# Kernel optimization log

Measured on AMD Instinct MI355X. Metric: run time of the kernel, lower is better.

Reference implementation:

```python
import jax, jax.numpy as jnp
import numpy as np

# ---- static problem configuration (matches init_kwargs) ----
N_PAIRS = 256
NODES_PER_GRAPH = 64
EDGES_PER_GRAPH = 200
MAX_EDGES = 256            # max_edge_set_size
N_GRAPHS = 2 * N_PAIRS     # query/corpus interleaved
N_NODES = N_GRAPHS * NODES_PER_GRAPH
N_EDGES = N_GRAPHS * EDGES_PER_GRAPH
NODE_DIM = 16
EDGE_DIM = 16
H = 128                    # node_state_dim
E_ENC = 64                 # encoded edge feature dim
MSG = 256                  # edge_hidden_sizes[-1] = 2*H (GMN GRU convention)
SK = 32                    # sinkhorn_feature_dim
PROP_STEPS = 5
SK_ITERS = 20
TEMP = 0.1


def setup_inputs() -> dict:
    key = jax.random.key(0)
    ks = jax.random.split(key, 16)
    node_features = jax.random.normal(ks[0], (N_NODES, NODE_DIM), jnp.float32)
    edge_features = jax.random.normal(ks[1], (N_EDGES, EDGE_DIM), jnp.float32)
    # edges are grouped per graph (graph g owns edges [g*E, (g+1)*E)) and
    # endpoints stay inside graph g's node range, as get_graph_features assumes
    offs = np.repeat(np.arange(N_GRAPHS) * NODES_PER_GRAPH, EDGES_PER_GRAPH)
    rng = np.random.default_rng(0)
    from_idx = jnp.asarray(offs + rng.integers(0, NODES_PER_GRAPH, N_EDGES), jnp.int32)
    to_idx = jnp.asarray(offs + rng.integers(0, NODES_PER_GRAPH, N_EDGES), jnp.int32)

    def lin(k, i, o):
        return jax.random.normal(k, (i, o), jnp.float32) / np.sqrt(i).astype(np.float32)

    p = dict(
        enc_node_w=lin(ks[2], NODE_DIM, H), enc_node_b=jnp.zeros((H,), jnp.float32),
        enc_edge_w=lin(ks[3], EDGE_DIM, E_ENC), enc_edge_b=jnp.zeros((E_ENC,), jnp.float32),
        msg_w1=lin(ks[4], 2 * H + E_ENC, MSG), msg_b1=jnp.zeros((MSG,), jnp.float32),
        msg_w2=lin(ks[5], MSG, MSG), msg_b2=jnp.zeros((MSG,), jnp.float32),
        rmsg_w1=lin(ks[6], 2 * H + E_ENC, MSG), rmsg_b1=jnp.zeros((MSG,), jnp.float32),
        rmsg_w2=lin(ks[7], MSG, MSG), rmsg_b2=jnp.zeros((MSG,), jnp.float32),
        gru_w_ih=lin(ks[8], MSG, 3 * H), gru_b_ih=jnp.zeros((3 * H,), jnp.float32),
        gru_w_hh=lin(ks[9], H, 3 * H), gru_b_hh=jnp.zeros((3 * H,), jnp.float32),
        sk_w1=lin(ks[10], MSG, SK), sk_b1=jnp.zeros((SK,), jnp.float32),
        sk_w2=lin(ks[11], SK, SK), sk_b2=jnp.zeros((SK,), jnp.float32),
    )
    return {"node_features": node_features, "edge_features": edge_features,
            "from_idx": from_idx, "to_idx": to_idx, **p}


def _mlp2(x, w1, b1, w2, b2):
    # Linear -> ReLU -> Linear (GMN MLP: no activation after last layer)
    return jax.nn.relu(x @ w1 + b1) @ w2 + b2


def reference(node_features, edge_features, from_idx, to_idx,
              enc_node_w, enc_node_b, enc_edge_w, enc_edge_b,
              msg_w1, msg_b1, msg_w2, msg_b2,
              rmsg_w1, rmsg_b1, rmsg_w2, rmsg_b2,
              gru_w_ih, gru_b_ih, gru_w_hh, gru_b_hh,
              sk_w1, sk_b1, sk_w2, sk_b2):
    # ---- GraphEncoder (single-layer MLPs) ----
    h = node_features @ enc_node_w + enc_node_b          # [N_NODES, H]
    e = edge_features @ enc_edge_w + enc_edge_b          # [N_EDGES, E_ENC]

    def edge_msgs(h):
        s, d = h[from_idx], h[to_idx]                    # gathers [N_EDGES, H]
        fwd = _mlp2(jnp.concatenate([s, d, e], axis=1), msg_w1, msg_b1, msg_w2, msg_b2)
        rev = _mlp2(jnp.concatenate([d, s, e], axis=1), rmsg_w1, rmsg_b1, rmsg_w2, rmsg_b2)
        return fwd, rev                                  # [N_EDGES, MSG] each

    # ---- propagation loop: gather -> edge MLP -> scatter -> GRU update ----
    for _ in range(PROP_STEPS):
        fwd, rev = edge_msgs(h)
        agg = (jax.ops.segment_sum(fwd, to_idx, num_segments=N_NODES)
               + jax.ops.segment_sum(rev, from_idx, num_segments=N_NODES))  # [N_NODES, MSG]
        gi = agg @ gru_w_ih + gru_b_ih                   # [N_NODES, 3H]
        gh = h @ gru_w_hh + gru_b_hh
        r = jax.nn.sigmoid(gi[:, :H] + gh[:, :H])
        z = jax.nn.sigmoid(gi[:, H:2 * H] + gh[:, H:2 * H])
        n = jnp.tanh(gi[:, 2 * H:] + r * gh[:, 2 * H:])
        h = (1.0 - z) * n + z * h                        # torch GRU update

    # ---- propagation_messages: per-edge fwd + rev message ----
    fwd, rev = edge_msgs(h)
    e_final = fwd + rev                                  # [N_EDGES, MSG]

    # ---- split_and_stack: per-graph edge sets padded to MAX_EDGES ----
    stacked = jnp.pad(e_final.reshape(N_GRAPHS, EDGES_PER_GRAPH, MSG),
                      ((0, 0), (0, MAX_EDGES - EDGES_PER_GRAPH), (0, 0)))
    q, c = stacked[0::2], stacked[1::2]                  # [B, MAX_EDGES, MSG]

    # ---- sinkhorn feature MLP + size mask ----
    tq = _mlp2(q, sk_w1, sk_b1, sk_w2, sk_b2)            # [B, MAX_EDGES, SK]
    tc = _mlp2(c, sk_w1, sk_b1, sk_w2, sk_b2)
    mask = (jnp.arange(MAX_EDGES) < EDGES_PER_GRAPH).astype(jnp.float32)[None, :, None]
    mq, mc = mask * tq, mask * tc

    # ---- log-domain Sinkhorn ----
    la = jnp.einsum('bif,bjf->bij', mq, mc) / TEMP       # [B, MAX_EDGES, MAX_EDGES]
    for _ in range(SK_ITERS):
        la = la - jax.nn.logsumexp(la, axis=2, keepdims=True)
        la = la - jax.nn.logsumexp(la, axis=1, keepdims=True)
    plan = jnp.exp(la)

    # ---- feature_alignment_score: -sum relu(q - P @ c) ----
    return -jnp.sum(jax.nn.relu(q - jnp.einsum('bij,bjf->bif', plan, c)), axis=(1, 2))
```

## Files before the change

### kernel.cpp

```cpp
#include <hip/hip_runtime.h>
#include <math.h>

typedef __attribute__((ext_vector_type(4))) float f32x4;
typedef __attribute__((ext_vector_type(8))) short s16x8;
typedef __attribute__((ext_vector_type(4))) short s16x4;

#define NN 32768
#define NE 102400
#define HD 128
#define EED 64
#define MSGD 256
#define NG 512
#define EPG 200
#define NP 256
#define SKD 32

__device__ inline short f2bf(float x){
  union{float f; unsigned u;} z; z.f=x;
  unsigned r = (z.u + 0x7fffu + ((z.u>>16)&1u)) >> 16;
  return (short)r;
}
__device__ inline float bf2f(unsigned short u){
  union{unsigned u; float f;} z; z.u = ((unsigned)u)<<16; return z.f;
}
__device__ inline float frcp(float x){
  float r; asm("v_rcp_f32 %0, %1" : "=v"(r) : "v"(x)); return r;
}

__global__ void __launch_bounds__(256) k_enc_node(const float* __restrict__ nf,
    const float* __restrict__ W, const float* __restrict__ b,
    float* __restrict__ h, short* __restrict__ hb){
  __shared__ float Ws[16*128];
  int t = threadIdx.x;
  for (int i=t;i<16*128;i+=256) Ws[i]=W[i];
  __syncthreads();
  int node = blockIdx.x*2 + (t>>7);
  int f = t & 127;
  const float* x = nf + node*16;
  float acc = b[f];
  #pragma unroll
  for (int k=0;k<16;k++) acc = fmaf(x[k], Ws[k*128+f], acc);
  h[node*HD+f] = acc;
  hb[node*HD+f] = f2bf(acc);
}

__global__ void __launch_bounds__(256) k_enc_edge(const float* __restrict__ ef,
    const float* __restrict__ W, const float* __restrict__ b, short* __restrict__ eeb){
  __shared__ float Ws[16*64];
  int t = threadIdx.x;
  for (int i=t;i<16*64;i+=256) Ws[i]=W[i];
  __syncthreads();
  int edge = blockIdx.x*4 + (t>>6);
  int f = t & 63;
  const float* x = ef + edge*16;
  float acc = b[f];
  #pragma unroll
  for (int k=0;k<16;k++) acc = fmaf(x[k], Ws[k*64+f], acc);
  eeb[edge*EED+f] = f2bf(acc);
}

__global__ void __launch_bounds__(256) k_pack(const float* __restrict__ W,
    short* __restrict__ dst, int K, int N){
  int NT = N >> 4;
  int i = blockIdx.x*256 + threadIdx.x;
  if (i >= (K/32)*NT*64) return;
  int l = i & 63, tile = i >> 6;
  int nt = tile % NT, kt = tile / NT;
  int lr = l & 15, lq = l >> 4;
  s16x8 v;
  #pragma unroll
  for (int j=0;j<8;j++)
    v[j] = f2bf(W[(size_t)(kt*32 + lq*8 + j)*N + nt*16 + lr]);
  *((s16x8*)dst + i) = v;
}

__global__ void __launch_bounds__(256) k_csr_count(const int* __restrict__ fidx,
    const int* __restrict__ tidx, int* __restrict__ cur_in, int* __restrict__ cur_out){
  int e = blockIdx.x*256 + threadIdx.x;
  if (e >= NE) return;
  atomicAdd(&cur_in[tidx[e]], 1);
  atomicAdd(&cur_out[fidx[e]], 1);
}
__global__ void k_csr_scan(int* __restrict__ cur_in, int* __restrict__ start_in,
    int* __restrict__ cur_out, int* __restrict__ start_out){
  if (threadIdx.x) return;
  int g = blockIdx.x;
  int n0 = g*64, base = g*EPG;
  int run = base;
  for (int i=0;i<64;i++){ int c=cur_in[n0+i]; start_in[n0+i]=run; cur_in[n0+i]=run; run+=c; }
  run = base;
  for (int i=0;i<64;i++){ int c=cur_out[n0+i]; start_out[n0+i]=run; cur_out[n0+i]=run; run+=c; }
}
__global__ void __launch_bounds__(256) k_csr_fill(const int* __restrict__ fidx,
    const int* __restrict__ tidx, int* __restrict__ cur_in, int* __restrict__ cur_out,
    int* __restrict__ list_in, int* __restrict__ list_out){
  int e = blockIdx.x*256 + threadIdx.x;
  if (e >= NE) return;
  int p1 = atomicAdd(&cur_in[tidx[e]], 1);  list_in[p1] = e;
  int p2 = atomicAdd(&cur_out[fidx[e]], 1); list_out[p2] = e;
}

template<bool FIN>
__global__ void __launch_bounds__(512,4) k_msg(const short* __restrict__ hb,
    const short* __restrict__ eeb, const int* __restrict__ from_idx, const int* __restrict__ to_idx,
    const short* __restrict__ w1f, const float* __restrict__ b1f,
    const short* __restrict__ w2f, const float* __restrict__ b2f,
    const short* __restrict__ w1r, const float* __restrict__ b1r,
    const short* __restrict__ w2r, const float* __restrict__ b2r,
    short* __restrict__ mf, short* __restrict__ mr){
  __shared__ __align__(16) short Xs[64][328];
  __shared__ __align__(16) short Ys[64][264];
  __shared__ int sidx[64], didx[64];
  int t = threadIdx.x;
  int e0 = blockIdx.x*64;
  if (t < 64){ sidx[t]=from_idx[e0+t]; didx[t]=to_idx[e0+t]; }
  __syncthreads();
  for (int i=t; i<64*40; i+=512){
    int r = i/40, c8 = (i - r*40)*8;
    const short* src;
    if (c8 < 128)      src = hb + (size_t)sidx[r]*HD + c8;
    else if (c8 < 256) src = hb + (size_t)didx[r]*HD + (c8-128);
    else               src = eeb + (size_t)(e0+r)*EED + (c8-256);
    *(s16x8*)&Xs[r][c8] = *(const s16x8*)src;
  }
  __syncthreads();

  int wv = t>>6, l = t&63, lr = l&15, lq = l>>4;
  int cbase = wv*32;
  f32x4 fsv[4][2];

  for (int dir=0; dir<2; dir++){
    const s16x8* W1v = (const s16x8*)(dir ? w1r : w1f);
    const float* B1  = dir ? b1r : b1f;
    const s16x8* W2v = (const s16x8*)(dir ? w2r : w2f);
    const float* B2  = dir ? b2r : b2f;

    f32x4 acc[4][2];
    #pragma unroll
    for (int ct=0; ct<2; ct++){
      float bb = B1[cbase + ct*16 + lr];
      #pragma unroll
      for (int rt=0; rt<4; rt++) acc[rt][ct] = (f32x4){bb,bb,bb,bb};
    }
    {
      s16x8 a0[4], b0[2], b1[2];
      int sc0 = dir ? 4 : 0;
      #pragma unroll
      for (int rt=0;rt<4;rt++) a0[rt] = *(const s16x8*)&Xs[rt*16+lr][sc0*32 + lq*8];
      #pragma unroll
      for (int ct=0;ct<2;ct++) b0[ct] = W1v[(size_t)(0*16 + wv*2 + ct)*64 + l];
      #pragma unroll
      for (int ct=0;ct<2;ct++) b1[ct] = W1v[(size_t)(1*16 + wv*2 + ct)*64 + l];
      #pragma unroll
      for (int kt=0; kt<10; kt++){
        s16x8 an[4], bn[2];
        if (kt < 9){
          int sc = (dir && (kt+1)<8) ? ((kt+1)^4) : (kt+1);
          #pragma unroll
          for (int rt=0;rt<4;rt++) an[rt] = *(const s16x8*)&Xs[rt*16+lr][sc*32 + lq*8];
        }
        if (kt < 8){
          #pragma unroll
          for (int ct=0;ct<2;ct++) bn[ct] = W1v[(size_t)((kt+2)*16 + wv*2 + ct)*64 + l];
        }
        #pragma unroll
        for (int rt=0; rt<4; rt++)
          #pragma unroll
          for (int ct=0; ct<2; ct++)
            acc[rt][ct] = __builtin_amdgcn_mfma_f32_16x16x32_bf16(a0[rt], b0[ct], acc[rt][ct], 0,0,0);
        #pragma unroll
        for (int i=0;i<4;i++) a0[i]=an[i];
        #pragma unroll
        for (int i=0;i<2;i++){ b0[i]=b1[i]; b1[i]=bn[i]; }
      }
    }
    #pragma unroll
    for (int rt=0; rt<4; rt++)
      #pragma unroll
      for (int ct=0; ct<2; ct++)
        #pragma unroll
        for (int r=0; r<4; r++)
          Ys[rt*16 + lq*4 + r][cbase + ct*16 + lr] = f2bf(fmaxf(acc[rt][ct][r], 0.f));
    __syncthreads();

    f32x4 acc2[4][2];
    #pragma unroll
    for (int ct=0; ct<2; ct++){
      float bb = B2[cbase + ct*16 + lr];
      #pragma unroll
      for (int rt=0; rt<4; rt++) acc2[rt][ct] = (f32x4){bb,bb,bb,bb};
    }
    {
      s16x8 a0[4], b0[2], b1[2];
      #pragma unroll
      for (int rt=0;rt<4;rt++) a0[rt] = *(const s16x8*)&Ys[rt*16+lr][lq*8];
      #pragma unroll
      for (int ct=0;ct<2;ct++) b0[ct] = W2v[(size_t)(0*16 + wv*2 + ct)*64 + l];
      #pragma unroll
      for (int ct=0;ct<2;ct++) b1[ct] = W2v[(size_t)(1*16 + wv*2 + ct)*64 + l];
      #pragma unroll
      for (int kt=0; kt<8; kt++){
        s16x8 an[4], bn[2];
        if (kt < 7){
          #pragma unroll
          for (int rt=0;rt<4;rt++) an[rt] = *(const s16x8*)&Ys[rt*16+lr][(kt+1)*32 + lq*8];
        }
        if (kt < 6){
          #pragma unroll
          for (int ct=0;ct<2;ct++) bn[ct] = W2v[(size_t)((kt+2)*16 + wv*2 + ct)*64 + l];
        }
        #pragma unroll
        for (int rt=0; rt<4; rt++)
          #pragma unroll
          for (int ct=0; ct<2; ct++)
            acc2[rt][ct] = __builtin_amdgcn_mfma_f32_16x16x32_bf16(a0[rt], b0[ct], acc2[rt][ct], 0,0,0);
        #pragma unroll
        for (int i=0;i<4;i++) a0[i]=an[i];
        #pragma unroll
        for (int i=0;i<2;i++){ b0[i]=b1[i]; b1[i]=bn[i]; }
      }
    }
    if (!FIN){
      __syncthreads();
      #pragma unroll
      for (int rt=0; rt<4; rt++)
        #pragma unroll
        for (int ct=0; ct<2; ct++)
          #pragma unroll
          for (int r=0; r<4; r++)
            Ys[rt*16 + lq*4 + r][cbase + ct*16 + lr] = f2bf(acc2[rt][ct][r]);
      __syncthreads();
      short* dst = (dir ? mr : mf) + (size_t)e0*MSGD;
      for (int i=t; i<64*32; i+=512){
        int row = i>>5, c8 = (i&31)*8;
        *(s16x8*)&dst[(size_t)row*MSGD + c8] = *(const s16x8*)&Ys[row][c8];
      }
      __syncthreads();
    } else {
      if (dir==0){
        #pragma unroll
        for (int rt=0; rt<4; rt++)
          #pragma unroll
          for (int ct=0; ct<2; ct++) fsv[rt][ct] = acc2[rt][ct];
        __syncthreads();
      } else {
        __syncthreads();
        #pragma unroll
        for (int rt=0; rt<4; rt++)
          #pragma unroll
          for (int ct=0; ct<2; ct++)
            #pragma unroll
            for (int r=0; r<4; r++)
              Ys[rt*16 + lq*4 + r][cbase + ct*16 + lr] = f2bf(fsv[rt][ct][r] + acc2[rt][ct][r]);
        __syncthreads();
        short* dst = mf + (size_t)e0*MSGD;
        for (int i=t; i<64*32; i+=512){
          int row = i>>5, c8 = (i&31)*8;
          *(s16x8*)&dst[(size_t)row*MSGD + c8] = *(const s16x8*)&Ys[row][c8];
        }
      }
    }
  }
}

__global__ void __launch_bounds__(256) k_gather(const unsigned short* __restrict__ mf,
    const unsigned short* __restrict__ mr,
    const int* __restrict__ start_in, const int* __restrict__ end_in, const int* __restrict__ list_in,
    const int* __restrict__ start_out, const int* __restrict__ end_out, const int* __restrict__ list_out,
    short* __restrict__ aggb){
  int n = blockIdx.x*4 + (threadIdx.x>>6);
  int l = threadIdx.x & 63;
  float4 acc = {0.f,0.f,0.f,0.f};
  int s0 = start_in[n], e0 = end_in[n];
  for (int i=s0; i<e0; i++){
    int e = list_in[i];
    ushort4 v = *(const ushort4*)&mf[(size_t)e*MSGD + 4*l];
    acc.x += bf2f(v.x); acc.y += bf2f(v.y); acc.z += bf2f(v.z); acc.w += bf2f(v.w);
  }
  int s1 = start_out[n], e1 = end_out[n];
  for (int i=s1; i<e1; i++){
    int e = list_out[i];
    ushort4 v = *(const ushort4*)&mr[(size_t)e*MSGD + 4*l];
    acc.x += bf2f(v.x); acc.y += bf2f(v.y); acc.z += bf2f(v.z); acc.w += bf2f(v.w);
  }
  s16x4 o;
  o[0]=f2bf(acc.x); o[1]=f2bf(acc.y); o[2]=f2bf(acc.z); o[3]=f2bf(acc.w);
  *(s16x4*)&aggb[(size_t)n*MSGD + 4*l] = o;
}

__global__ void __launch_bounds__(512,4) k_gru(const float* __restrict__ h,
    const short* __restrict__ hb, const short* __restrict__ aggb,
    const short* __restrict__ wih_p, const float* __restrict__ bih,
    const short* __restrict__ whh_p, const float* __restrict__ bhh,
    float* __restrict__ hnew, short* __restrict__ hnewb){
  __shared__ __align__(16) short aggs[64][264];
  __shared__ __align__(16) short hs[64][136];
  int t = threadIdx.x;
  int n0 = blockIdx.x*64;
  for (int i=t; i<64*32; i+=512){
    int r = i>>5, c8 = (i&31)*8;
    *(s16x8*)&aggs[r][c8] = *(const s16x8*)&aggb[(size_t)(n0+r)*MSGD + c8];
  }
  for (int i=t; i<64*16; i+=512){
    int r = i>>4, c8 = (i&15)*8;
    *(s16x8*)&hs[r][c8] = *(const s16x8*)&hb[(size_t)(n0+r)*HD + c8];
  }
  __syncthreads();

  int wv = t>>6, l = t&63, lr = l&15, lq = l>>4;
  const s16x8* Wih_v = (const s16x8*)wih_p;
  const s16x8* Whh_v = (const s16x8*)whh_p;

  f32x4 gi[4][3], gh[4][3];
  #pragma unroll
  for (int ct=0; ct<3; ct++){
    int bcol = ct*128 + wv*16 + lr;
    float bi = bih[bcol], bh = bhh[bcol];
    #pragma unroll
    for (int rt=0; rt<4; rt++){
      gi[rt][ct] = (f32x4){bi,bi,bi,bi};
      gh[rt][ct] = (f32x4){bh,bh,bh,bh};
    }
  }
  for (int kt=0; kt<8; kt++){
    s16x8 af[4], bfr[3];
    #pragma unroll
    for (int rt=0; rt<4; rt++) af[rt] = *(const s16x8*)&aggs[rt*16+lr][kt*32 + lq*8];
    #pragma unroll
    for (int ct=0; ct<3; ct++)
      bfr[ct] = Wih_v[(size_t)(kt*24 + ct*8 + wv)*64 + l];
    #pragma unroll
    for (int rt=0; rt<4; rt++)
      #pragma unroll
      for (int ct=0; ct<3; ct++)
        gi[rt][ct] = __builtin_amdgcn_mfma_f32_16x16x32_bf16(af[rt], bfr[ct], gi[rt][ct], 0,0,0);
  }
  for (int kt=0; kt<4; kt++){
    s16x8 af[4], bfr[3];
    #pragma unroll
    for (int rt=0; rt<4; rt++) af[rt] = *(const s16x8*)&hs[rt*16+lr][kt*32 + lq*8];
    #pragma unroll
    for (int ct=0; ct<3; ct++)
      bfr[ct] = Whh_v[(size_t)(kt*24 + ct*8 + wv)*64 + l];
    #pragma unroll
    for (int rt=0; rt<4; rt++)
      #pragma unroll
      for (int ct=0; ct<3; ct++)
        gh[rt][ct] = __builtin_amdgcn_mfma_f32_16x16x32_bf16(af[rt], bfr[ct], gh[rt][ct], 0,0,0);
  }
  #pragma unroll
  for (int rt=0; rt<4; rt++)
    #pragma unroll
    for (int r=0; r<4; r++){
      int row = n0 + rt*16 + lq*4 + r;
      int col = wv*16 + lr;
      float rr = 1.f/(1.f + __expf(-(gi[rt][0][r] + gh[rt][0][r])));
      float zz = 1.f/(1.f + __expf(-(gi[rt][1][r] + gh[rt][1][r])));
      float gn = gi[rt][2][r] + rr*gh[rt][2][r];
      float nn = 1.f - 2.f/(__expf(2.f*gn) + 1.f);
      float hold = h[(size_t)row*HD + col];
      float hv = (1.f - zz)*nn + zz*hold;
      hnew[(size_t)row*HD + col] = hv;
      hnewb[(size_t)row*HD + col] = f2bf(hv);
    }
}

__global__ void __launch_bounds__(256,2) k_tall(const short* __restrict__ efb,
    const short* __restrict__ W1p, const float* __restrict__ b1,
    const short* __restrict__ W2p, const float* __restrict__ b2,
    float* __restrict__ tall){
  __shared__ __align__(16) short Xs[64][264];
  __shared__ __align__(16) short Ys[64][40];
  int t = threadIdx.x;
  int g = blockIdx.x>>2, r0 = (blockIdx.x&3)*64;
  for (int i=t; i<64*32; i+=256){
    int r = i>>5, c8 = (i&31)*8;
    int row = r0 + r;
    s16x8 v = (row < EPG) ? *(const s16x8*)&efb[((size_t)g*EPG + row)*MSGD + c8]
                          : (s16x8){0,0,0,0,0,0,0,0};
    *(s16x8*)&Xs[r][c8] = v;
  }
  __syncthreads();
  int wv = t>>6, l = t&63, lr = l&15, lq = l>>4;
  const s16x8* W1v = (const s16x8*)W1p;
  const s16x8* W2v = (const s16x8*)W2p;
  f32x4 acc[2];
  #pragma unroll
  for (int ct=0; ct<2; ct++){
    float bb = b1[ct*16 + lr];
    acc[ct] = (f32x4){bb,bb,bb,bb};
  }
  for (int kt=0; kt<8; kt++){
    s16x8 a = *(const s16x8*)&Xs[wv*16+lr][kt*32 + lq*8];
    #pragma unroll
    for (int ct=0; ct<2; ct++){
      s16x8 bfr = W1v[(size_t)(kt*2 + ct)*64 + l];
      acc[ct] = __builtin_amdgcn_mfma_f32_16x16x32_bf16(a, bfr, acc[ct], 0,0,0);
    }
  }
  #pragma unroll
  for (int ct=0; ct<2; ct++)
    #pragma unroll
    for (int r=0; r<4; r++)
      Ys[wv*16 + lq*4 + r][ct*16 + lr] = f2bf(fmaxf(acc[ct][r], 0.f));
  __syncthreads();
  f32x4 acc2[2];
  #pragma unroll
  for (int ct=0; ct<2; ct++){
    float bb = b2[ct*16 + lr];
    acc2[ct] = (f32x4){bb,bb,bb,bb};
  }
  {
    s16x8 a = *(const s16x8*)&Ys[wv*16+lr][lq*8];
    #pragma unroll
    for (int ct=0; ct<2; ct++){
      s16x8 bfr = W2v[(size_t)ct*64 + l];
      acc2[ct] = __builtin_amdgcn_mfma_f32_16x16x32_bf16(a, bfr, acc2[ct], 0,0,0);
    }
  }
  #pragma unroll
  for (int ct=0; ct<2; ct++)
    #pragma unroll
    for (int r=0; r<4; r++){
      int row = r0 + wv*16 + lq*4 + r;
      tall[((size_t)g*256 + row)*SKD + ct*16 + lr] = (row < EPG) ? acc2[ct][r] : 0.f;
    }
}

__global__ void __attribute__((amdgpu_waves_per_eu(4,4))) __launch_bounds__(1024)
k_sinkhorn(const float* __restrict__ tall, short* __restrict__ plan){
  __shared__ float tqs[256*32];
  __shared__ float tcsT[32*257];
  __shared__ float cv[256];
  __shared__ float psm[16][256];
  int p = blockIdx.x, t = threadIdx.x;
  int w = t>>6, l = t&63;
  int rbase = w*16;
  const float* tq = tall + (size_t)(2*p)*8192;
  const float* tc = tall + (size_t)(2*p+1)*8192;
  for (int i=t; i<8192; i+=1024){
    tqs[i] = tq[i];
    tcsT[(i&31)*257 + (i>>5)] = tc[i];
  }
  __syncthreads();
  float4 E[16];
  #pragma unroll
  for (int k=0; k<16; k++){
    float4 a = {0.f,0.f,0.f,0.f};
    for (int kk=0; kk<32; kk+=4){
      float4 c0 = *(const float4*)&tcsT[(kk+0)*257 + 4*l];
      float4 c1 = *(const float4*)&tcsT[(kk+1)*257 + 4*l];
      float4 c2 = *(const float4*)&tcsT[(kk+2)*257 + 4*l];
      float4 c3 = *(const float4*)&tcsT[(kk+3)*257 + 4*l];
      float4 q = *(const float4*)&tqs[(rbase+k)*32 + kk];
      a.x = fmaf(q.x,c0.x, fmaf(q.y,c1.x, fmaf(q.z,c2.x, fmaf(q.w,c3.x, a.x))));
      a.y = fmaf(q.x,c0.y, fmaf(q.y,c1.y, fmaf(q.z,c2.y, fmaf(q.w,c3.y, a.y))));
      a.z = fmaf(q.x,c0.z, fmaf(q.y,c1.z, fmaf(q.z,c2.z, fmaf(q.w,c3.z, a.z))));
      a.w = fmaf(q.x,c0.w, fmaf(q.y,c1.w, fmaf(q.z,c2.w, fmaf(q.w,c3.w, a.w))));
    }
    a.x *= 10.f; a.y *= 10.f; a.z *= 10.f; a.w *= 10.f;
    float m = fmaxf(fmaxf(a.x,a.y), fmaxf(a.z,a.w));
    #pragma unroll
    for (int off=32; off; off>>=1) m = fmaxf(m, __shfl_xor(m, off));
    float s = __expf(a.x-m)+__expf(a.y-m)+__expf(a.z-m)+__expf(a.w-m);
    #pragma unroll
    for (int off=32; off; off>>=1) s += __shfl_xor(s, off);
    float r = m + __logf(s);
    E[k].x = __expf(a.x - r); E[k].y = __expf(a.y - r);
    E[k].z = __expf(a.z - r); E[k].w = __expf(a.w - r);
  }

  for (int it=0; it<20; it++){
    float4 sm = {0.f,0.f,0.f,0.f};
    #pragma unroll
    for (int k=0;k<16;k++){
      sm.x += E[k].x; sm.y += E[k].y; sm.z += E[k].z; sm.w += E[k].w;
    }
    *(float4*)&psm[w][4*l] = sm;
    __syncthreads();
    if (t < 256){
      float s = psm[0][t];
      #pragma unroll
      for (int ww=1; ww<16; ww++) s += psm[ww][t];
      cv[t] = frcp(s);
    }
    __syncthreads();
    float4 ic = *(const float4*)&cv[4*l];
    #pragma unroll
    for (int k=0;k<16;k++){
      E[k].x *= ic.x; E[k].y *= ic.y; E[k].z *= ic.z; E[k].w *= ic.w;
    }
    if (it < 19){
      #pragma unroll
      for (int k=0;k<16;k++){
        float s = E[k].x + E[k].y + E[k].z + E[k].w;
        #pragma unroll
        for (int off=32; off; off>>=1) s += __shfl_xor(s, off);
        float inv = frcp(s);
        E[k].x *= inv; E[k].y *= inv; E[k].z *= inv; E[k].w *= inv;
      }
    }
  }
  short* P = plan + (size_t)p*65536;
  #pragma unroll
  for (int k=0;k<16;k++){
    s16x4 o;
    o[0]=f2bf(E[k].x); o[1]=f2bf(E[k].y); o[2]=f2bf(E[k].z); o[3]=f2bf(E[k].w);
    *(s16x4*)&P[(size_t)(rbase+k)*256 + 4*l] = o;
  }
}

__global__ void __launch_bounds__(256,2) k_loss(const short* __restrict__ plan,
    const short* __restrict__ efb, float* __restrict__ out){
  __shared__ __align__(16) short Ps[128][40];
  __shared__ __align__(16) short Cs[256][40];
  __shared__ float red[4];
  int t = threadIdx.x;
  int b = blockIdx.x, p = b>>1, rh = b&1;
  int i0 = rh*128;
  int wv = t>>6, l = t&63, lr = l&15, lq = l>>4;
  const short* Pb = plan + (size_t)p*65536;
  const unsigned short* C = (const unsigned short*)(efb + (size_t)(2*p+1)*EPG*MSGD);
  const unsigned short* Q = (const unsigned short*)(efb + (size_t)(2*p)*EPG*MSGD);

  f32x4 acc[2][16];
  #pragma unroll
  for (int rt=0;rt<2;rt++)
    #pragma unroll
    for (int ct=0;ct<16;ct++) acc[rt][ct] = (f32x4){0.f,0.f,0.f,0.f};

  for (int kt=0; kt<8; kt++){
    __syncthreads();
    for (int i=t; i<128*4; i+=256){
      int r = i>>2, c8 = (i&3)*8;
      *(s16x8*)&Ps[r][c8] = *(const s16x8*)&Pb[(size_t)(i0+r)*256 + kt*32 + c8];
    }
    for (int i=t; i<32*64; i+=256){
      int k = i>>6, c4 = (i&63)*4;
      int j = kt*32 + k;
      ushort4 v = (j < EPG) ? *(const ushort4*)&C[(size_t)j*256 + c4] : (ushort4){0,0,0,0};
      Cs[c4+0][k]=(short)v.x; Cs[c4+1][k]=(short)v.y; Cs[c4+2][k]=(short)v.z; Cs[c4+3][k]=(short)v.w;
    }
    __syncthreads();
    s16x8 a0 = *(const s16x8*)&Ps[wv*32      + lr][lq*8];
    s16x8 a1 = *(const s16x8*)&Ps[wv*32 + 16 + lr][lq*8];
    #pragma unroll
    for (int ct=0; ct<16; ct++){
      s16x8 bfr = *(const s16x8*)&Cs[ct*16+lr][lq*8];
      acc[0][ct] = __builtin_amdgcn_mfma_f32_16x16x32_bf16(a0, bfr, acc[0][ct], 0,0,0);
      acc[1][ct] = __builtin_amdgcn_mfma_f32_16x16x32_bf16(a1, bfr, acc[1][ct], 0,0,0);
    }
  }
  float s = 0.f;
  #pragma unroll
  for (int rt=0; rt<2; rt++)
    #pragma unroll
    for (int ct=0; ct<16; ct++)
      #pragma unroll
      for (int r=0; r<4; r++){
        int row = i0 + wv*32 + rt*16 + lq*4 + r;
        int col = ct*16 + lr;
        float q = (row < EPG) ? bf2f(Q[(size_t)row*256 + col]) : 0.f;
        s += fmaxf(q - acc[rt][ct][r], 0.f);
      }
  #pragma unroll
  for (int off=32; off; off>>=1) s += __shfl_xor(s, off);
  if (l==0) red[wv] = s;
  __syncthreads();
  if (t==0) atomicAdd(&out[p], -(red[0]+red[1]+red[2]+red[3]));
}

extern "C" void kernel_launch(void* const* d_in, const int* in_sizes, int n_in,
                              void* d_out, int out_size, void* d_ws, size_t ws_size,
                              hipStream_t stream){
  const float* nf   = (const float*)d_in[0];
  const float* ef   = (const float*)d_in[1];
  const int*   fidx = (const int*)d_in[2];
  const int*   tidx = (const int*)d_in[3];
  const float* enw  = (const float*)d_in[4];
  const float* enb  = (const float*)d_in[5];
  const float* eew  = (const float*)d_in[6];
  const float* eeb_w= (const float*)d_in[7];
  const float* mw1  = (const float*)d_in[8];
  const float* mb1  = (const float*)d_in[9];
  const float* mw2  = (const float*)d_in[10];
  const float* mb2  = (const float*)d_in[11];
  const float* rw1  = (const float*)d_in[12];
  const float* rb1  = (const float*)d_in[13];
  const float* rw2  = (const float*)d_in[14];
  const float* rb2  = (const float*)d_in[15];
  const float* wih  = (const float*)d_in[16];
  const float* bih  = (const float*)d_in[17];
  const float* whh  = (const float*)d_in[18];
  const float* bhh  = (const float*)d_in[19];
  const float* skw1 = (const float*)d_in[20];
  const float* skb1 = (const float*)d_in[21];
  const float* skw2 = (const float*)d_in[22];
  const float* skb2 = (const float*)d_in[23];
  float* out = (float*)d_out;

  float* ws = (float*)d_ws;
  float* h_a   = ws;
  float* h_b   = h_a + (size_t)NN*HD;
  short* hb_a  = (short*)(h_b + (size_t)NN*HD);
  short* hb_b  = hb_a + (size_t)NN*HD;
  short* ee_b  = hb_b + (size_t)NN*HD;
  short* mf    = ee_b + (size_t)NE*EED;
  short* mr    = mf + (size_t)NE*MSGD;
  short* e_finb = mf;
  float* t_all = (float*)(mr + (size_t)NE*MSGD);
  float* la    = t_all + (size_t)NG*256*SKD;

  short* w1f_p = (short*)t_all;
  short* w1r_p = w1f_p + 320*256;
  short* w2f_p = w1r_p + 320*256;
  short* w2r_p = w2f_p + 256*256;
  short* wih_p = w2r_p + 256*256;
  short* whh_p = wih_p + 256*384;
  int*   csr   = (int*)(t_all + 221184);
  int* cur_in    = csr;
  int* cur_out   = cur_in  + NN;
  int* start_in  = cur_out + NN;
  int* start_out = start_in + NN;
  int* list_in   = start_out + NN;
  int* list_out  = list_in + NE;

  short* aggb   = (short*)la;
  short* plan_s = (short*)la;
  short* skw1_p = (short*)(la + 9000000);
  short* skw2_p = skw1_p + 256*32;

  k_pack<<<40, 256, 0, stream>>>(mw1, w1f_p, 320, 256);
  k_pack<<<40, 256, 0, stream>>>(rw1, w1r_p, 320, 256);
  k_pack<<<32, 256, 0, stream>>>(mw2, w2f_p, 256, 256);
  k_pack<<<32, 256, 0, stream>>>(rw2, w2r_p, 256, 256);
  k_pack<<<48, 256, 0, stream>>>(wih, wih_p, 256, 384);
  k_pack<<<24, 256, 0, stream>>>(whh, whh_p, 128, 384);
  k_pack<<<4, 256, 0, stream>>>(skw1, skw1_p, 256, 32);
  k_pack<<<1, 256, 0, stream>>>(skw2, skw2_p, 32, 32);

  k_enc_node<<<NN/2, 256, 0, stream>>>(nf, enw, enb, h_a, hb_a);
  k_enc_edge<<<NE/4, 256, 0, stream>>>(ef, eew, eeb_w, ee_b);

  hipMemsetAsync(csr, 0, (size_t)2*NN*sizeof(int), stream);
  k_csr_count<<<NE/256, 256, 0, stream>>>(fidx, tidx, cur_in, cur_out);
  k_csr_scan<<<NG, 64, 0, stream>>>(cur_in, start_in, cur_out, start_out);
  k_csr_fill<<<NE/256, 256, 0, stream>>>(fidx, tidx, cur_in, cur_out, list_in, list_out);

  float* hc = h_a; float* hn = h_b;
  short* hbc = hb_a; short* hbn = hb_b;
  for (int step=0; step<5; step++){
    k_msg<false><<<NE/64, 512, 0, stream>>>(hbc, ee_b, fidx, tidx,
        w1f_p, mb1, w2f_p, mb2, w1r_p, rb1, w2r_p, rb2, mf, mr);
    k_gather<<<NN/4, 256, 0, stream>>>((const unsigned short*)mf, (const unsigned short*)mr,
        start_in, cur_in, list_in, start_out, cur_out, list_out, aggb);
    k_gru<<<NN/64, 512, 0, stream>>>(hc, hbc, aggb, wih_p, bih, whh_p, bhh, hn, hbn);
    float* tmp = hc; hc = hn; hn = tmp;
    short* tmb = hbc; hbc = hbn; hbn = tmb;
  }
  k_msg<true><<<NE/64, 512, 0, stream>>>(hbc, ee_b, fidx, tidx,
      w1f_p, mb1, w2f_p, mb2, w1r_p, rb1, w2r_p, rb2, e_finb, mr);

  k_tall<<<NG*4, 256, 0, stream>>>(e_finb, skw1_p, skb1, skw2_p, skb2, t_all);
  k_sinkhorn<<<NP, 1024, 0, stream>>>(t_all, plan_s);

  hipMemsetAsync(out, 0, (size_t)NP*sizeof(float), stream);
  k_loss<<<NP*2, 256, 0, stream>>>(plan_s, e_finb, out);
}
```

Measured before the change: 1.094 ms.

## Halve msg/GRU block threads, widen per-wave tiles, gather A directly from global

```diff
diff --git a/kernel.cpp b/kernel.cpp
--- a/kernel.cpp
+++ b/kernel.cpp
@@ -101,33 +101,29 @@
 }
 
 template<bool FIN>
-__global__ void __launch_bounds__(512,4) k_msg(const short* __restrict__ hb,
+__global__ void __launch_bounds__(256, FIN?2:3) k_msg(const short* __restrict__ hb,
     const short* __restrict__ eeb, const int* __restrict__ from_idx, const int* __restrict__ to_idx,
     const short* __restrict__ w1f, const float* __restrict__ b1f,
     const short* __restrict__ w2f, const float* __restrict__ b2f,
     const short* __restrict__ w1r, const float* __restrict__ b1r,
     const short* __restrict__ w2r, const float* __restrict__ b2r,
-    short* __restrict__ mf, short* __restrict__ mr){
-  __shared__ __align__(16) short Xs[64][328];
+    short* __restrict__ out0, short* __restrict__ out1){
   __shared__ __align__(16) short Ys[64][264];
-  __shared__ int sidx[64], didx[64];
   int t = threadIdx.x;
   int e0 = blockIdx.x*64;
-  if (t < 64){ sidx[t]=from_idx[e0+t]; didx[t]=to_idx[e0+t]; }
-  __syncthreads();
-  for (int i=t; i<64*40; i+=512){
-    int r = i/40, c8 = (i - r*40)*8;
-    const short* src;
-    if (c8 < 128)      src = hb + (size_t)sidx[r]*HD + c8;
-    else if (c8 < 256) src = hb + (size_t)didx[r]*HD + (c8-128);
-    else               src = eeb + (size_t)(e0+r)*EED + (c8-256);
-    *(s16x8*)&Xs[r][c8] = *(const s16x8*)src;
-  }
-  __syncthreads();
-
   int wv = t>>6, l = t&63, lr = l&15, lq = l>>4;
-  int cbase = wv*32;
-  f32x4 fsv[4][2];
+  int cbase = wv*64;
+
+  int hs_off[4], hd_off[4], ee_off[4];
+  #pragma unroll
+  for (int rt=0; rt<4; rt++){
+    int row = e0 + rt*16 + lr;
+    hs_off[rt] = from_idx[row]*HD;
+    hd_off[rt] = to_idx[row]*HD;
+    ee_off[rt] = row*EED;
+  }
+
+  f32x4 fsv[4][4];
 
   for (int dir=0; dir<2; dir++){
     const s16x8* W1v = (const s16x8*)(dir ? w1r : w1f);
@@ -135,129 +131,116 @@
     const s16x8* W2v = (const s16x8*)(dir ? w2r : w2f);
     const float* B2  = dir ? b2r : b2f;
 
-    f32x4 acc[4][2];
-    #pragma unroll
-    for (int ct=0; ct<2; ct++){
+    f32x4 acc[4][4];
+    #pragma unroll
+    for (int ct=0; ct<4; ct++){
       float bb = B1[cbase + ct*16 + lr];
       #pragma unroll
       for (int rt=0; rt<4; rt++) acc[rt][ct] = (f32x4){bb,bb,bb,bb};
     }
     {
-      s16x8 a0[4], b0[2], b1[2];
-      int sc0 = dir ? 4 : 0;
-      #pragma unroll
-      for (int rt=0;rt<4;rt++) a0[rt] = *(const s16x8*)&Xs[rt*16+lr][sc0*32 + lq*8];
-      #pragma unroll
-      for (int ct=0;ct<2;ct++) b0[ct] = W1v[(size_t)(0*16 + wv*2 + ct)*64 + l];
-      #pragma unroll
-      for (int ct=0;ct<2;ct++) b1[ct] = W1v[(size_t)(1*16 + wv*2 + ct)*64 + l];
+      s16x8 b0[4];
+      #pragma unroll
+      for (int ct=0;ct<4;ct++) b0[ct] = W1v[(size_t)(0*16 + wv*4 + ct)*64 + l];
       #pragma unroll
       for (int kt=0; kt<10; kt++){
-        s16x8 an[4], bn[2];
+        s16x8 bn[4];
         if (kt < 9){
-          int sc = (dir && (kt+1)<8) ? ((kt+1)^4) : (kt+1);
           #pragma unroll
-          for (int rt=0;rt<4;rt++) an[rt] = *(const s16x8*)&Xs[rt*16+lr][sc*32 + lq*8];
+          for (int ct=0;ct<4;ct++) bn[ct] = W1v[(size_t)((kt+1)*16 + wv*4 + ct)*64 + l];
         }
-        if (kt < 8){
-          #pragma unroll
-          for (int ct=0;ct<2;ct++) bn[ct] = W1v[(size_t)((kt+2)*16 + wv*2 + ct)*64 + l];
+        s16x8 a0[4];
+        #pragma unroll
+        for (int rt=0; rt<4; rt++){
+          const short* ap;
+          if (kt < 4){
+            int off = dir ? hd_off[rt] : hs_off[rt];
+            ap = hb + off + kt*32 + lq*8;
+          } else if (kt < 8){
+            int off = dir ? hs_off[rt] : hd_off[rt];
+            ap = hb + off + (kt-4)*32 + lq*8;
+          } else {
+            ap = eeb + ee_off[rt] + (kt-8)*32 + lq*8;
+          }
+          a0[rt] = *(const s16x8*)ap;
         }
         #pragma unroll
         for (int rt=0; rt<4; rt++)
           #pragma unroll
-          for (int ct=0; ct<2; ct++)
+          for (int ct=0; ct<4; ct++)
             acc[rt][ct] = __builtin_amdgcn_mfma_f32_16x16x32_bf16(a0[rt], b0[ct], acc[rt][ct], 0,0,0);
         #pragma unroll
-        for (int i=0;i<4;i++) a0[i]=an[i];
-        #pragma unroll
-        for (int i=0;i<2;i++){ b0[i]=b1[i]; b1[i]=bn[i]; }
+        for (int i=0;i<4;i++) b0[i]=bn[i];
       }
     }
+    if (dir==1) __syncthreads();
     #pragma unroll
     for (int rt=0; rt<4; rt++)
       #pragma unroll
-      for (int ct=0; ct<2; ct++)
+      for (int ct=0; ct<4; ct++)
         #pragma unroll
         for (int r=0; r<4; r++)
           Ys[rt*16 + lq*4 + r][cbase + ct*16 + lr] = f2bf(fmaxf(acc[rt][ct][r], 0.f));
     __syncthreads();
 
-    f32x4 acc2[4][2];
-    #pragma unroll
-    for (int ct=0; ct<2; ct++){
+    f32x4 acc2[4][4];
+    #pragma unroll
+    for (int ct=0; ct<4; ct++){
       float bb = B2[cbase + ct*16 + lr];
       #pragma unroll
       for (int rt=0; rt<4; rt++) acc2[rt][ct] = (f32x4){bb,bb,bb,bb};
     }
     {
-      s16x8 a0[4], b0[2], b1[2];
-      #pragma unroll
-      for (int rt=0;rt<4;rt++) a0[rt] = *(const s16x8*)&Ys[rt*16+lr][lq*8];
-      #pragma unroll
-      for (int ct=0;ct<2;ct++) b0[ct] = W2v[(size_t)(0*16 + wv*2 + ct)*64 + l];
-      #pragma unroll
-      for (int ct=0;ct<2;ct++) b1[ct] = W2v[(size_t)(1*16 + wv*2 + ct)*64 + l];
+      s16x8 b0[4];
+      #pragma unroll
+      for (int ct=0;ct<4;ct++) b0[ct] = W2v[(size_t)(0*16 + wv*4 + ct)*64 + l];
       #pragma unroll
       for (int kt=0; kt<8; kt++){
-        s16x8 an[4], bn[2];
+        s16x8 bn[4];
         if (kt < 7){
           #pragma unroll
-          for (int rt=0;rt<4;rt++) an[rt] = *(const s16x8*)&Ys[rt*16+lr][(kt+1)*32 + lq*8];
+          for (int ct=0;ct<4;ct++) bn[ct] = W2v[(size_t)((kt+1)*16 + wv*4 + ct)*64 + l];
         }
-        if (kt < 6){
-          #pragma unroll
-          for (int ct=0;ct<2;ct++) bn[ct] = W2v[(size_t)((kt+2)*16 + wv*2 + ct)*64 + l];
-        }
+        s16x8 a0[4];
+        #pragma unroll
+        for (int rt=0;rt<4;rt++) a0[rt] = *(const s16x8*)&Ys[rt*16+lr][kt*32 + lq*8];
         #pragma unroll
         for (int rt=0; rt<4; rt++)
           #pragma unroll
-          for (int ct=0; ct<2; ct++)
+          for (int ct=0; ct<4; ct++)
             acc2[rt][ct] = __builtin_amdgcn_mfma_f32_16x16x32_bf16(a0[rt], b0[ct], acc2[rt][ct], 0,0,0);
         #pragma unroll
-        for (int i=0;i<4;i++) a0[i]=an[i];
-        #pragma unroll
-        for (int i=0;i<2;i++){ b0[i]=b1[i]; b1[i]=bn[i]; }
+        for (int i=0;i<4;i++) b0[i]=bn[i];
       }
     }
+
     if (!FIN){
-      __syncthreads();
+      short* dst = (dir ? out1 : out0);
       #pragma unroll
       for (int rt=0; rt<4; rt++)
         #pragma unroll
-        for (int ct=0; ct<2; ct++)
+        for (int ct=0; ct<4; ct++)
           #pragma unroll
-          for (int r=0; r<4; r++)
-            Ys[rt*16 + lq*4 + r][cbase + ct*16 + lr] = f2bf(acc2[rt][ct][r]);
-      __syncthreads();
-      short* dst = (dir ? mr : mf) + (size_t)e0*MSGD;
-      for (int i=t; i<64*32; i+=512){
-        int row = i>>5, c8 = (i&31)*8;
-        *(s16x8*)&dst[(size_t)row*MSGD + c8] = *(const s16x8*)&Ys[row][c8];
-      }
-      __syncthreads();
+          for (int r=0; r<4; r++){
+            int row = e0 + rt*16 + lq*4 + r;
+            dst[(size_t)row*MSGD + cbase + ct*16 + lr] = f2bf(acc2[rt][ct][r]);
+          }
     } else {
       if (dir==0){
         #pragma unroll
         for (int rt=0; rt<4; rt++)
           #pragma unroll
-          for (int ct=0; ct<2; ct++) fsv[rt][ct] = acc2[rt][ct];
-        __syncthreads();
+          for (int ct=0; ct<4; ct++) fsv[rt][ct] = acc2[rt][ct];
       } else {
-        __syncthreads();
         #pragma unroll
         for (int rt=0; rt<4; rt++)
           #pragma unroll
-          for (int ct=0; ct<2; ct++)
+          for (int ct=0; ct<4; ct++)
             #pragma unroll
-            for (int r=0; r<4; r++)
-              Ys[rt*16 + lq*4 + r][cbase + ct*16 + lr] = f2bf(fsv[rt][ct][r] + acc2[rt][ct][r]);
-        __syncthreads();
-        short* dst = mf + (size_t)e0*MSGD;
-        for (int i=t; i<64*32; i+=512){
-          int row = i>>5, c8 = (i&31)*8;
-          *(s16x8*)&dst[(size_t)row*MSGD + c8] = *(const s16x8*)&Ys[row][c8];
-        }
+            for (int r=0; r<4; r++){
+              int row = e0 + rt*16 + lq*4 + r;
+              out0[(size_t)row*MSGD + cbase + ct*16 + lr] = f2bf(fsv[rt][ct][r] + acc2[rt][ct][r]);
+            }
       }
     }
   }
@@ -288,7 +271,7 @@
   *(s16x4*)&aggb[(size_t)n*MSGD + 4*l] = o;
 }
 
-__global__ void __launch_bounds__(512,4) k_gru(const float* __restrict__ h,
+__global__ void __launch_bounds__(256,2) k_gru(const float* __restrict__ h,
     const short* __restrict__ hb, const short* __restrict__ aggb,
     const short* __restrict__ wih_p, const float* __restrict__ bih,
     const short* __restrict__ whh_p, const float* __restrict__ bhh,
@@ -297,11 +280,11 @@
   __shared__ __align__(16) short hs[64][136];
   int t = threadIdx.x;
   int n0 = blockIdx.x*64;
-  for (int i=t; i<64*32; i+=512){
+  for (int i=t; i<64*32; i+=256){
     int r = i>>5, c8 = (i&31)*8;
     *(s16x8*)&aggs[r][c8] = *(const s16x8*)&aggb[(size_t)(n0+r)*MSGD + c8];
   }
-  for (int i=t; i<64*16; i+=512){
+  for (int i=t; i<64*16; i+=256){
     int r = i>>4, c8 = (i&15)*8;
     *(s16x8*)&hs[r][c8] = *(const s16x8*)&hb[(size_t)(n0+r)*HD + c8];
   }
@@ -311,10 +294,10 @@
   const s16x8* Wih_v = (const s16x8*)wih_p;
   const s16x8* Whh_v = (const s16x8*)whh_p;
 
-  f32x4 gi[4][3], gh[4][3];
-  #pragma unroll
-  for (int ct=0; ct<3; ct++){
-    int bcol = ct*128 + wv*16 + lr;
+  f32x4 gi[4][6], gh[4][6];
+  #pragma unroll
+  for (int ct=0; ct<6; ct++){
+    int bcol = (ct>>1)*128 + wv*32 + (ct&1)*16 + lr;
     float bi = bih[bcol], bh = bhh[bcol];
     #pragma unroll
     for (int rt=0; rt<4; rt++){
@@ -323,46 +306,52 @@
     }
   }
   for (int kt=0; kt<8; kt++){
-    s16x8 af[4], bfr[3];
+    s16x8 af[4], bfr[6];
     #pragma unroll
     for (int rt=0; rt<4; rt++) af[rt] = *(const s16x8*)&aggs[rt*16+lr][kt*32 + lq*8];
     #pragma unroll
-    for (int ct=0; ct<3; ct++)
-      bfr[ct] = Wih_v[(size_t)(kt*24 + ct*8 + wv)*64 + l];
+    for (int ct=0; ct<6; ct++){
+      int nt = (ct>>1)*8 + wv*2 + (ct&1);
+      bfr[ct] = Wih_v[(size_t)(kt*24 + nt)*64 + l];
+    }
     #pragma unroll
     for (int rt=0; rt<4; rt++)
       #pragma unroll
-      for (int ct=0; ct<3; ct++)
+      for (int ct=0; ct<6; ct++)
         gi[rt][ct] = __builtin_amdgcn_mfma_f32_16x16x32_bf16(af[rt], bfr[ct], gi[rt][ct], 0,0,0);
   }
   for (int kt=0; kt<4; kt++){
-    s16x8 af[4], bfr[3];
+    s16x8 af[4], bfr[6];
     #pragma unroll
     for (int rt=0; rt<4; rt++) af[rt] = *(const s16x8*)&hs[rt*16+lr][kt*32 + lq*8];
     #pragma unroll
-    for (int ct=0; ct<3; ct++)
-      bfr[ct] = Whh_v[(size_t)(kt*24 + ct*8 + wv)*64 + l];
+    for (int ct=0; ct<6; ct++){
+      int nt = (ct>>1)*8 + wv*2 + (ct&1);
+      bfr[ct] = Whh_v[(size_t)(kt*24 + nt)*64 + l];
+    }
     #pragma unroll
     for (int rt=0; rt<4; rt++)
       #pragma unroll
-      for (int ct=0; ct<3; ct++)
+      for (int ct=0; ct<6; ct++)
         gh[rt][ct] = __builtin_amdgcn_mfma_f32_16x16x32_bf16(af[rt], bfr[ct], gh[rt][ct], 0,0,0);
   }
   #pragma unroll
   for (int rt=0; rt<4; rt++)
     #pragma unroll
-    for (int r=0; r<4; r++){
-      int row = n0 + rt*16 + lq*4 + r;
-      int col = wv*16 + lr;
-      float rr = 1.f/(1.f + __expf(-(gi[rt][0][r] + gh[rt][0][r])));
-      float zz = 1.f/(1.f + __expf(-(gi[rt][1][r] + gh[rt][1][r])));
-      float gn = gi[rt][2][r] + rr*gh[rt][2][r];
-      float nn = 1.f - 2.f/(__expf(2.f*gn) + 1.f);
-      float hold = h[(size_t)row*HD + col];
-      float hv = (1.f - zz)*nn + zz*hold;
-      hnew[(size_t)row*HD + col] = hv;
-      hnewb[(size_t)row*HD + col] = f2bf(hv);
-    }
+    for (int j=0; j<2; j++)
+      #pragma unroll
+      for (int r=0; r<4; r++){
+        int row = n0 + rt*16 + lq*4 + r;
+        int col = wv*32 + j*16 + lr;
+        float rr = 1.f/(1.f + __expf(-(gi[rt][j][r]   + gh[rt][j][r])));
+        float zz = 1.f/(1.f + __expf(-(gi[rt][2+j][r] + gh[rt][2+j][r])));
+        float gn = gi[rt][4+j][r] + rr*gh[rt][4+j][r];
+        float nn = 1.f - 2.f/(__expf(2.f*gn) + 1.f);
+        float hold = h[(size_t)row*HD + col];
+        float hv = (1.f - zz)*nn + zz*hold;
+        hnew[(size_t)row*HD + col] = hv;
+        hnewb[(size_t)row*HD + col] = f2bf(hv);
+      }
 }
 
 __global__ void __launch_bounds__(256,2) k_tall(const short* __restrict__ efb,
@@ -445,29 +434,48 @@
   __syncthreads();
   float4 E[16];
   #pragma unroll
-  for (int k=0; k<16; k++){
-    float4 a = {0.f,0.f,0.f,0.f};
+  for (int kg=0; kg<4; kg++){
+    float4 a0_ = {0.f,0.f,0.f,0.f}, a1_ = a0_, a2_ = a0_, a3_ = a0_;
     for (int kk=0; kk<32; kk+=4){
       float4 c0 = *(const float4*)&tcsT[(kk+0)*257 + 4*l];
       float4 c1 = *(const float4*)&tcsT[(kk+1)*257 + 4*l];
       float4 c2 = *(const float4*)&tcsT[(kk+2)*257 + 4*l];
       float4 c3 = *(const float4*)&tcsT[(kk+3)*257 + 4*l];
-      float4 q = *(const float4*)&tqs[(rbase+k)*32 + kk];
-      a.x = fmaf(q.x,c0.x, fmaf(q.y,c1.x, fmaf(q.z,c2.x, fmaf(q.w,c3.x, a.x))));
-      a.y = fmaf(q.x,c0.y, fmaf(q.y,c1.y, fmaf(q.z,c2.y, fmaf(q.w,c3.y, a.y))));
-      a.z = fmaf(q.x,c0.z, fmaf(q.y,c1.z, fmaf(q.z,c2.z, fmaf(q.w,c3.z, a.z))));
-      a.w = fmaf(q.x,c0.w, fmaf(q.y,c1.w, fmaf(q.z,c2.w, fmaf(q.w,c3.w, a.w))));
-    }
-    a.x *= 10.f; a.y *= 10.f; a.z *= 10.f; a.w *= 10.f;
-    float m = fmaxf(fmaxf(a.x,a.y), fmaxf(a.z,a.w));
-    #pragma unroll
-    for (int off=32; off; off>>=1) m = fmaxf(m, __shfl_xor(m, off));
-    float s = __expf(a.x-m)+__expf(a.y-m)+__expf(a.z-m)+__expf(a.w-m);
-    #pragma unroll
-    for (int off=32; off; off>>=1) s += __shfl_xor(s, off);
-    float r = m + __logf(s);
-    E[k].x = __expf(a.x - r); E[k].y = __expf(a.y - r);
-    E[k].z = __expf(a.z - r); E[k].w = __expf(a.w - r);
+      float4 q0 = *(const float4*)&tqs[(rbase+kg*4+0)*32 + kk];
+      float4 q1 = *(const float4*)&tqs[(rbase+kg*4+1)*32 + kk];
+      float4 q2 = *(const float4*)&tqs[(rbase+kg*4+2)*32 + kk];
+      float4 q3 = *(const float4*)&tqs[(rbase+kg*4+3)*32 + kk];
+      a0_.x = fmaf(q0.x,c0.x, fmaf(q0.y,c1.x, fmaf(q0.z,c2.x, fmaf(q0.w,c3.x, a0_.x))));
+      a0_.y = fmaf(q0.x,c0.y, fmaf(q0.y,c1.y, fmaf(q0.z,c2.y, fmaf(q0.w,c3.y, a0_.y))));
+      a0_.z = fmaf(q0.x,c0.z, fmaf(q0.y,c1.z, fmaf(q0.z,c2.z, fmaf(q0.w,c3.z, a0_.z))));
+      a0_.w = fmaf(q0.x,c0.w, fmaf(q0.y,c1.w, fmaf(q0.z,c2.w, fmaf(q0.w,c3.w, a0_.w))));
+      a1_.x = fmaf(q1.x,c0.x, fmaf(q1.y,c1.x, fmaf(q1.z,c2.x, fmaf(q1.w,c3.x, a1_.x))));
+      a1_.y = fmaf(q1.x,c0.y, fmaf(q1.y,c1.y, fmaf(q1.z,c2.y, fmaf(q1.w,c3.y, a1_.y))));
+      a1_.z = fmaf(q1.x,c0.z, fmaf(q1.y,c1.z, fmaf(q1.z,c2.z, fmaf(q1.w,c3.z, a1_.z))));
+      a1_.w = fmaf(q1.x,c0.w, fmaf(q1.y,c1.w, fmaf(q1.z,c2.w, fmaf(q1.w,c3.w, a1_.w))));
+      a2_.x = fmaf(q2.x,c0.x, fmaf(q2.y,c1.x, fmaf(q2.z,c2.x, fmaf(q2.w,c3.x, a2_.x))));
+      a2_.y = fmaf(q2.x,c0.y, fmaf(q2.y,c1.y, fmaf(q2.z,c2.y, fmaf(q2.w,c3.y, a2_.y))));
+      a2_.z = fmaf(q2.x,c0.z, fmaf(q2.y,c1.z, fmaf(q2.z,c2.z, fmaf(q2.w,c3.z, a2_.z))));
+      a2_.w = fmaf(q2.x,c0.w, fmaf(q2.y,c1.w, fmaf(q2.z,c2.w, fmaf(q2.w,c3.w, a2_.w))));
+      a3_.x = fmaf(q3.x,c0.x, fmaf(q3.y,c1.x, fmaf(q3.z,c2.x, fmaf(q3.w,c3.x, a3_.x))));
+      a3_.y = fmaf(q3.x,c0.y, fmaf(q3.y,c1.y, fmaf(q3.z,c2.y, fmaf(q3.w,c3.y, a3_.y))));
+      a3_.z = fmaf(q3.x,c0.z, fmaf(q3.y,c1.z, fmaf(q3.z,c2.z, fmaf(q3.w,c3.z, a3_.z))));
+      a3_.w = fmaf(q3.x,c0.w, fmaf(q3.y,c1.w, fmaf(q3.z,c2.w, fmaf(q3.w,c3.w, a3_.w))));
+    }
+    #pragma unroll
+    for (int j=0; j<4; j++){
+      float4 a = (j==0)?a0_:(j==1)?a1_:(j==2)?a2_:a3_;
+      a.x *= 10.f; a.y *= 10.f; a.z *= 10.f; a.w *= 10.f;
+      float m = fmaxf(fmaxf(a.x,a.y), fmaxf(a.z,a.w));
+      #pragma unroll
+      for (int off=32; off; off>>=1) m = fmaxf(m, __shfl_xor(m, off));
+      float s = __expf(a.x-m)+__expf(a.y-m)+__expf(a.z-m)+__expf(a.w-m);
+      #pragma unroll
+      for (int off=32; off; off>>=1) s += __shfl_xor(s, off);
+      float r = m + __logf(s);
+      E[kg*4+j].x = __expf(a.x - r); E[kg*4+j].y = __expf(a.y - r);
+      E[kg*4+j].z = __expf(a.z - r); E[kg*4+j].w = __expf(a.w - r);
+    }
   }
 
   for (int it=0; it<20; it++){
@@ -650,15 +658,15 @@
   float* hc = h_a; float* hn = h_b;
   short* hbc = hb_a; short* hbn = hb_b;
   for (int step=0; step<5; step++){
-    k_msg<false><<<NE/64, 512, 0, stream>>>(hbc, ee_b, fidx, tidx,
+    k_msg<false><<<NE/64, 256, 0, stream>>>(hbc, ee_b, fidx, tidx,
         w1f_p, mb1, w2f_p, mb2, w1r_p, rb1, w2r_p, rb2, mf, mr);
     k_gather<<<NN/4, 256, 0, stream>>>((const unsigned short*)mf, (const unsigned short*)mr,
         start_in, cur_in, list_in, start_out, cur_out, list_out, aggb);
-    k_gru<<<NN/64, 512, 0, stream>>>(hc, hbc, aggb, wih_p, bih, whh_p, bhh, hn, hbn);
+    k_gru<<<NN/64, 256, 0, stream>>>(hc, hbc, aggb, wih_p, bih, whh_p, bhh, hn, hbn);
     float* tmp = hc; hc = hn; hn = tmp;
     short* tmb = hbc; hbc = hbn; hbn = tmb;
   }
-  k_msg<true><<<NE/64, 512, 0, stream>>>(hbc, ee_b, fidx, tidx,
+  k_msg<true><<<NE/64, 256, 0, stream>>>(hbc, ee_b, fidx, tidx,
       w1f_p, mb1, w2f_p, mb2, w1r_p, rb1, w2r_p, rb2, e_finb, mr);
 
   k_tall<<<NG*4, 256, 0, stream>>>(e_finb, skw1_p, skb1, skw2_p, skb2, t_all);
```

Result: slower. 1.511 ms (+38.0%).
